# Kernel optimization log

Measured on AMD Instinct MI355X. Metric: run time of the kernel, lower is better.

## Reference

```python
import jax, jax.numpy as jnp
import numpy as np

IOU_THR = 0.0  # module calls batched NMS with iou_threshold=0.0


def setup_inputs() -> dict:
    key = jax.random.key(0)
    kx, kc, kr = jax.random.split(key, 3)
    return {
        "x": jax.random.normal(kx, (10,), jnp.float32),
        "c": jax.random.normal(kc, (4,), jnp.float32),   # learned param
        "r": jax.random.normal(kr, (10,), jnp.float32),  # learned param
    }


def _pairwise_iou(b):
    # b: [n,4] (x1,y1,x2,y2); torchvision-style IoU (area not clamped, inter clamped at 0)
    x1, y1, x2, y2 = b[:, 0], b[:, 1], b[:, 2], b[:, 3]
    area = (x2 - x1) * (y2 - y1)
    iw = jnp.maximum(jnp.minimum(x2[:, None], x2[None, :]) - jnp.maximum(x1[:, None], x1[None, :]), 0.0)
    ih = jnp.maximum(jnp.minimum(y2[:, None], y2[None, :]) - jnp.maximum(y1[:, None], y1[None, :]), 0.0)
    inter = iw * ih
    return inter / (area[:, None] + area[None, :] - inter)


def _nms(boxes, scores, thr):
    # returns (order, keep_mask_in_sorted_order), fixed shapes (jit-safe)
    n = boxes.shape[0]
    order = jnp.argsort(-scores)
    iou = _pairwise_iou(boxes[order])
    j = jnp.arange(n)

    def body(i, keep):
        sup = (iou[i] > thr) & keep[i] & (j > i)
        return keep & ~sup

    keep = jax.lax.fori_loop(0, n, body, jnp.ones((n,), bool))
    return order, keep


def reference(x, c, r):
    boxes = jnp.outer(x, c)                      # [10,4]
    scores = r * x                               # [10]
    # batched-NMS coordinate trick: idxs = arange -> each box in its own class
    max_coord = boxes.max()
    offsets = jnp.arange(boxes.shape[0], dtype=boxes.dtype) * (max_coord + 1.0)
    boxes_nms = boxes + offsets[:, None]
    order, keep = _nms(boxes_nms, scores, IOU_THR)
    # torch returns boxes[keep] (dynamic shape). With distinct class ids all boxes
    # survive; we return fixed-shape [10,4] in keep order, suppressed rows zeroed.
    return jnp.where(keep[:, None], boxes[order], 0.0)
```

## Files before the change

kernel.cpp:

```cpp
#include <hip/hip_runtime.h>
#include <math.h>

#define N 10
#define C 4

__global__ __launch_bounds__(64, 1)
void Model_78056735637556_kernel(const float* __restrict__ x,
                                 const float* __restrict__ c,
                                 const float* __restrict__ r,
                                 float* __restrict__ out) {
    __shared__ float s_boxes[N][C];
    __shared__ float s_scores[N];
    __shared__ int   s_order[N];
    __shared__ int   s_keep[N];

    const int t = threadIdx.x;

    if (t < N * C) {
        int i = t / C, k = t % C;
        s_boxes[i][k] = x[i] * c[k];
    }
    if (t < N) s_scores[t] = r[t] * x[t];
    __syncthreads();

    if (t == 0) {
        float maxc = -INFINITY;
        for (int i = 0; i < N; ++i)
            for (int k = 0; k < C; ++k) maxc = fmaxf(maxc, s_boxes[i][k]);

        int order[N];
        for (int i = 0; i < N; ++i) order[i] = i;
        for (int i = 1; i < N; ++i) {
            int oi = order[i];
            float s = s_scores[oi];
            int j = i - 1;
            while (j >= 0 && s_scores[order[j]] < s) {
                order[j + 1] = order[j];
                --j;
            }
            order[j + 1] = oi;
        }

        float off = maxc + 1.0f;
        float bn[N][C];
        float area[N];
        for (int i = 0; i < N; ++i) {
            int o = order[i];
            float d = (float)o * off;
            for (int k = 0; k < C; ++k) bn[i][k] = s_boxes[o][k] + d;
            area[i] = (bn[i][2] - bn[i][0]) * (bn[i][3] - bn[i][1]);
        }

        int keep[N];
        for (int i = 0; i < N; ++i) keep[i] = 1;
        for (int i = 0; i < N; ++i) {
            if (!keep[i]) continue;
            for (int j = i + 1; j < N; ++j) {
                float iw = fmaxf(fminf(bn[i][2], bn[j][2]) - fmaxf(bn[i][0], bn[j][0]), 0.0f);
                float ih = fmaxf(fminf(bn[i][3], bn[j][3]) - fmaxf(bn[i][1], bn[j][1]), 0.0f);
                float inter = iw * ih;
                float iou = inter / (area[i] + area[j] - inter);
                if (iou > 0.0f) keep[j] = 0;
            }
        }
        for (int i = 0; i < N; ++i) { s_order[i] = order[i]; s_keep[i] = keep[i]; }
    }
    __syncthreads();

    if (t < N * C) {
        int i = t / C, k = t % C;
        out[t] = s_keep[i] ? s_boxes[s_order[i]][k] : 0.0f;
    }
}

extern "C" void kernel_launch(void* const* d_in, const int* in_sizes, int n_in,
                              void* d_out, int out_size, void* d_ws, size_t ws_size,
                              hipStream_t stream) {
    const float* x = (const float*)d_in[0];
    const float* c = (const float*)d_in[1];
    const float* r = (const float*)d_in[2];
    float* out = (float*)d_out;
    Model_78056735637556_kernel<<<1, 64, 0, stream>>>(x, c, r, out);
}
```

Before: 62.50 us.

## Parallelize NMS sort and suppression across threads with rank sort

Result: faster. 59.37 us (-5.0%).

```diff
diff --git a/kernel.cpp b/kernel.cpp
--- a/kernel.cpp
+++ b/kernel.cpp
@@ -13,62 +13,65 @@
     __shared__ float s_scores[N];
     __shared__ int   s_order[N];
     __shared__ int   s_keep[N];
+    __shared__ float s_n[N][5];
 
     const int t = threadIdx.x;
+    const int i = t >> 2;
+    const int k = t & 3;
 
-    if (t < N * C) {
-        int i = t / C, k = t % C;
-        s_boxes[i][k] = x[i] * c[k];
-    }
-    if (t < N) s_scores[t] = r[t] * x[t];
+    if (t < N * C) s_boxes[i][k] = x[i] * c[k];
+    if (t < N) { s_scores[t] = r[t] * x[t]; s_keep[t] = 1; }
     __syncthreads();
 
-    if (t == 0) {
-        float maxc = -INFINITY;
-        for (int i = 0; i < N; ++i)
-            for (int k = 0; k < C; ++k) maxc = fmaxf(maxc, s_boxes[i][k]);
-
-        int order[N];
-        for (int i = 0; i < N; ++i) order[i] = i;
-        for (int i = 1; i < N; ++i) {
-            int oi = order[i];
-            float s = s_scores[oi];
-            int j = i - 1;
-            while (j >= 0 && s_scores[order[j]] < s) {
-                order[j + 1] = order[j];
-                --j;
-            }
-            order[j + 1] = oi;
+    if (t < N) {
+        const float s = s_scores[t];
+        int rank = 0;
+        #pragma unroll
+        for (int j = 0; j < N; ++j) {
+            const float sj = s_scores[j];
+            rank += (sj > s) || ((sj == s) && (j < t));
         }
-
-        float off = maxc + 1.0f;
-        float bn[N][C];
-        float area[N];
-        for (int i = 0; i < N; ++i) {
-            int o = order[i];
-            float d = (float)o * off;
-            for (int k = 0; k < C; ++k) bn[i][k] = s_boxes[o][k] + d;
-            area[i] = (bn[i][2] - bn[i][0]) * (bn[i][3] - bn[i][1]);
-        }
-
-        int keep[N];
-        for (int i = 0; i < N; ++i) keep[i] = 1;
-        for (int i = 0; i < N; ++i) {
-            if (!keep[i]) continue;
-            for (int j = i + 1; j < N; ++j) {
-                float iw = fmaxf(fminf(bn[i][2], bn[j][2]) - fmaxf(bn[i][0], bn[j][0]), 0.0f);
-                float ih = fmaxf(fminf(bn[i][3], bn[j][3]) - fmaxf(bn[i][1], bn[j][1]), 0.0f);
-                float inter = iw * ih;
-                float iou = inter / (area[i] + area[j] - inter);
-                if (iou > 0.0f) keep[j] = 0;
-            }
-        }
-        for (int i = 0; i < N; ++i) { s_order[i] = order[i]; s_keep[i] = keep[i]; }
+        s_order[rank] = t;
     }
     __syncthreads();
 
+    float n0 = 0.0f, n1 = 0.0f, n2 = 0.0f, n3 = 0.0f, ar = 0.0f;
+    if (t < N) {
+        float m = -INFINITY;
+        #pragma unroll
+        for (int ii = 0; ii < N; ++ii)
+            #pragma unroll
+            for (int kk = 0; kk < C; ++kk)
+                m = fmaxf(m, s_boxes[ii][kk]);
+        const float off = m + 1.0f;
+
+        const int o = s_order[t];
+        const float d = (float)o * off;
+        n0 = s_boxes[o][0] + d;
+        n1 = s_boxes[o][1] + d;
+        n2 = s_boxes[o][2] + d;
+        n3 = s_boxes[o][3] + d;
+        ar = (n2 - n0) * (n3 - n1);
+        s_n[t][0] = n0; s_n[t][1] = n1; s_n[t][2] = n2; s_n[t][3] = n3;
+        s_n[t][4] = ar;
+    }
+    __syncthreads();
+
+    #pragma unroll
+    for (int p = 0; p < N - 1; ++p) {
+        if (t > p && t < N) {
+            if (s_keep[p] && s_keep[t]) {
+                const float iw = fmaxf(fminf(s_n[p][2], n2) - fmaxf(s_n[p][0], n0), 0.0f);
+                const float ih = fmaxf(fminf(s_n[p][3], n3) - fmaxf(s_n[p][1], n1), 0.0f);
+                const float inter = iw * ih;
+                const float iou = inter / (s_n[p][4] + ar - inter);
+                if (iou > 0.0f) s_keep[t] = 0;
+            }
+        }
+        __syncthreads();
+    }
+
     if (t < N * C) {
-        int i = t / C, k = t % C;
         out[t] = s_keep[i] ? s_boxes[s_order[i]][k] : 0.0f;
     }
 }
```
